# Optimization experiments

Hardware: AMD Instinct MI355X
Metric: run time of the kernel (lower is better)

The kernel has to match this reference:

```python
import jax, jax.numpy as jnp
import numpy as np

N, E, D, C, NEG_SLOPE = 50000, 800000, 128, 40, 0.2


def setup_inputs() -> dict:
    key = jax.random.key(0)
    ks = jax.random.split(key, 20)
    inp = {
        'x': jax.random.normal(ks[0], (N, D), dtype=jnp.float32),
        'edge_index': jax.random.randint(ks[1], (2, E), 0, N, dtype=jnp.int64),
    }
    s = 1.0 / np.sqrt(D)
    for l in range(3):
        inp[f'W{l}'] = jax.random.normal(ks[2 + 4 * l], (D, D), dtype=jnp.float32) * s
        inp[f'a_src{l}'] = jax.random.normal(ks[3 + 4 * l], (D,), dtype=jnp.float32) * s
        inp[f'a_dst{l}'] = jax.random.normal(ks[4 + 4 * l], (D,), dtype=jnp.float32) * s
        inp[f'b{l}'] = jnp.zeros((D,), dtype=jnp.float32)
    inp['W_head'] = jax.random.normal(ks[14], (D, C), dtype=jnp.float32) * s
    inp['b_head'] = jnp.zeros((C,), dtype=jnp.float32)
    return inp


def gat_layer(x, src, dst, W, a_src, a_dst, b):
    # x: [N, D]; src/dst: [E+N] (self-loops included)
    h = x @ W                                   # [N, D] node transform
    e_s = h @ a_src                             # [N] source attention logits
    e_d = h @ a_dst                             # [N] dest attention logits
    alpha = jax.nn.leaky_relu(e_s[src] + e_d[dst], NEG_SLOPE)  # [E+N]
    # segment softmax over incoming edges of each dst node
    m = jax.ops.segment_max(alpha, dst, num_segments=N)
    ex = jnp.exp(alpha - m[dst])
    z = jax.ops.segment_sum(ex, dst, num_segments=N)
    w = ex / z[dst]                             # [E+N] normalized attention
    out = jax.ops.segment_sum(w[:, None] * h[src], dst, num_segments=N)
    return out + b


def reference(x, edge_index, W0, a_src0, a_dst0, b0, W1, a_src1, a_dst1, b1,
              W2, a_src2, a_dst2, b2, W_head, b_head):
    loops = jnp.arange(N, dtype=edge_index.dtype)
    src = jnp.concatenate([edge_index[0], loops])  # PyG add_self_loops=True
    dst = jnp.concatenate([edge_index[1], loops])
    for W, a_s, a_d, b in ((W0, a_src0, a_dst0, b0),
                           (W1, a_src1, a_dst1, b1),
                           (W2, a_src2, a_dst2, b2)):
        x = jax.nn.relu(gat_layer(x, src, dst, W, a_s, a_d, b))
        # dropout is identity in eval mode
    return x @ W_head + b_head
```

## Files before the change

kernel.cpp:

```cpp
#include <hip/hip_runtime.h>
#include <hip/hip_bf16.h>

#define NN 50000
#define EE 800000
#define DD 128
#define CC 40
#define NEG 0.2f
#define NPAD 50048
#define NB 782
#define CEDGES 2048
#define NSCAT 391
#define PADCAP 2048
#define DEGCAP 64

typedef _Float16 half8 __attribute__((ext_vector_type(8)));
typedef unsigned short ushort8 __attribute__((ext_vector_type(8)));
typedef float floatx4 __attribute__((ext_vector_type(4)));

__device__ __forceinline__ float lrelu(float a) { return a > 0.f ? a : NEG * a; }
__device__ __forceinline__ float bf2f(unsigned short u) {
    union { unsigned int i; float f; } v; v.i = (unsigned int)u << 16; return v.f;
}

__device__ __forceinline__ int edge_at(const void* ei, int i64, long long idx) {
    return i64 ? (int)((const long long*)ei)[idx] : ((const int*)ei)[idx];
}

struct ParamCvt {
    const void* src[11];
    int off[11];
    int total;
};

__global__ __launch_bounds__(256) void prep_kernel(ParamCvt a,
                                                   const void* __restrict__ x_raw,
                                                   const void* __restrict__ ei,
                                                   const void* __restrict__ W0,
                                                   const void* __restrict__ W1,
                                                   const void* __restrict__ W2,
                                                   int* __restrict__ flags,
                                                   int* __restrict__ cursor,
                                                   unsigned int* __restrict__ pairs,
                                                   float* __restrict__ params,
                                                   _Float16* __restrict__ wpack) {
    __shared__ int cnt[NB];
    __shared__ int loff[NB];
    __shared__ int gbase[NB];
    __shared__ unsigned int lp[CEDGES];
    __shared__ int wsum[4];
    __shared__ int carry;
    int t = threadIdx.x, lane = t & 63, wid = t >> 6;
    if (blockIdx.x < NSCAT) {
        unsigned int hi0 = ((const unsigned int*)ei)[2 * lane + 1];
        int i64 = (__ballot(hi0 != 0u) == 0ull) ? 1 : 0;
        for (int i = t; i < NB; i += 256) cnt[i] = 0;
        if (t == 0) carry = 0;
        __syncthreads();
        int base = blockIdx.x * CEDGES;
        int sreg[8], dreg[8];
        #pragma unroll
        for (int j = 0; j < 8; ++j) {
            int e = base + j * 256 + t;
            if (e < EE) {
                sreg[j] = edge_at(ei, i64, e);
                dreg[j] = edge_at(ei, i64, (long long)EE + e);
                atomicAdd(&cnt[dreg[j] >> 6], 1);
            } else { sreg[j] = -1; dreg[j] = -1; }
        }
        __syncthreads();
        for (int c0 = 0; c0 < NB; c0 += 256) {
            int i = c0 + t;
            int v = (i < NB) ? cnt[i] : 0;
            int x = v;
            #pragma unroll
            for (int o = 1; o < 64; o <<= 1) {
                int y = __shfl_up(x, o, 64);
                if (lane >= o) x += y;
            }
            if (lane == 63) wsum[wid] = x;
            __syncthreads();
            int carr = carry;
            int woff = 0;
            for (int w = 0; w < wid; ++w) woff += wsum[w];
            if (i < NB) loff[i] = carr + woff + x - v;
            __syncthreads();
            if (t == 0) carry = carr + wsum[0] + wsum[1] + wsum[2] + wsum[3];
            __syncthreads();
        }
        for (int i = t; i < NB; i += 256) {
            int c = cnt[i];
            gbase[i] = c ? atomicAdd(&cursor[i], c) : 0;
        }
        __syncthreads();
        for (int i = t; i < NB; i += 256) cnt[i] = loff[i];
        __syncthreads();
        #pragma unroll
        for (int j = 0; j < 8; ++j) {
            if (dreg[j] >= 0) {
                int slot = atomicAdd(&cnt[dreg[j] >> 6], 1);
                lp[slot] = ((unsigned int)dreg[j] << 16) | (unsigned int)sreg[j];
            }
        }
        __syncthreads();
        int total = (EE - base < CEDGES) ? (EE - base) : CEDGES;
        for (int i = t; i < total; i += 256) {
            unsigned int pr = lp[i];
            int b = (int)(pr >> 22);
            int idx = gbase[b] + (i - loff[b]);
            if (idx < PADCAP)
                __builtin_nontemporal_store(pr, &pairs[(size_t)b * PADCAP + idx]);
        }
        return;
    }
    int cb = blockIdx.x - NSCAT;
    unsigned short u = ((const unsigned short*)x_raw)[lane * 2];
    int e = (u >> 7) & 0xFF;
    int bad = (!(e >= 96 && e <= 158) && u != 0 && u != 0x8000) ? 1 : 0;
    int bf = (__ballot(bad) == 0ull) ? 1 : 0;
    if (cb == 217) {
        unsigned int hi = ((const unsigned int*)ei)[2 * lane + 1];
        int i64 = (__ballot(hi != 0u) == 0ull) ? 1 : 0;
        if (t == 0) { flags[0] = bf; flags[1] = i64; }
        return;
    }
    if (cb < 192) {
        int i = cb * 256 + t;
        int l = i >> 14, r = i & 16383;
        int j = r & 7, ln = (r >> 3) & 63, ks = (r >> 9) & 3, c = r >> 11;
        int k = ks * 32 + (ln >> 4) * 8 + j;
        int ncol = c * 16 + (ln & 15);
        const void* W = (l == 0) ? W0 : ((l == 1) ? W1 : W2);
        float v = bf ? bf2f(((const unsigned short*)W)[k * 128 + ncol])
                     : ((const float*)W)[k * 128 + ncol];
        wpack[i] = (_Float16)v;
    } else {
        int i = (cb - 192) * 256 + t;
        if (i >= a.total) return;
        int k = 0;
        #pragma unroll
        for (int j = 1; j < 11; ++j) if (i >= a.off[j]) k = j;
        int local = i - a.off[k];
        params[i] = bf ? bf2f(((const unsigned short*)a.src[k])[local])
                       : ((const float*)a.src[k])[local];
    }
}

__device__ __forceinline__ void gemm_core(const half8 a[4], const _Float16* __restrict__ lw,
                                          const float* __restrict__ asrc,
                                          const float* __restrict__ adst,
                                          _Float16* __restrict__ H,
                                          float* __restrict__ es, float* __restrict__ ed,
                                          int n, int rowbase, int lane) {
    int quad = lane >> 4, col = lane & 15;
    float esp[4] = {0, 0, 0, 0}, edp[4] = {0, 0, 0, 0};
    #pragma unroll
    for (int c = 0; c < 8; ++c) {
        floatx4 acc = {0.f, 0.f, 0.f, 0.f};
        #pragma unroll
        for (int ks = 0; ks < 4; ++ks) {
            half8 b = *(const half8*)&lw[(((c * 4 + ks) * 64) + lane) * 8];
            acc = __builtin_amdgcn_mfma_f32_16x16x32_f16(a[ks], b, acc, 0, 0, 0);
        }
        float av = asrc[c * 16 + col], dv = adst[c * 16 + col];
        #pragma unroll
        for (int r = 0; r < 4; ++r) {
            int rowg = rowbase + quad * 4 + r;
            if (rowg < n) H[(size_t)rowg * 128 + c * 16 + col] = (_Float16)acc[r];
            esp[r] += acc[r] * av;
            edp[r] += acc[r] * dv;
        }
    }
    #pragma unroll
    for (int r = 0; r < 4; ++r) {
        float s = esp[r], d = edp[r];
        #pragma unroll
        for (int o = 1; o < 16; o <<= 1) {
            s += __shfl_xor(s, o, 64);
            d += __shfl_xor(d, o, 64);
        }
        int rowg = rowbase + quad * 4 + r;
        if (col == 0 && rowg < n) { es[rowg] = s; ed[rowg] = d; }
    }
}

__device__ __forceinline__ void agg_body(const _Float16* __restrict__ H,
                                         const int* __restrict__ cnt,
                                         const unsigned short* __restrict__ csr,
                                         const float* __restrict__ es,
                                         const float* __restrict__ ed,
                                         const float* __restrict__ bias,
                                         _Float16* __restrict__ Xout,
                                         int n, int blk64, int t) {
    int sub = t & 15, g = t >> 4;
    int f0 = sub * 8;
    #pragma unroll 1
    for (int r = 0; r < 4; ++r) {
        int node = blk64 + r * 16 + g;
        if (node >= n) continue;
        int total = cnt[node];
        size_t beg = (size_t)node << 6;
        float edi = ed[node];
        float wself = __expf(lrelu(es[node] + edi));
        float z = wself;
        half8 hs = *(const half8*)&H[(size_t)node * 128 + f0];
        float acc[8];
        #pragma unroll
        for (int j = 0; j < 8; ++j) acc[j] = wself * (float)hs[j];
        for (int base = 0; base < total; base += 8) {
            ushort8 c8 = *(const ushort8*)&csr[beg + base];
            int sdx[8];
            #pragma unroll
            for (int d = 0; d < 8; ++d)
                sdx[d] = (base + d < total) ? (int)c8[d] : node;
            half8 h[8];
            #pragma unroll
            for (int d = 0; d < 8; ++d)
                h[d] = *(const half8*)&H[(size_t)sdx[d] * 128 + f0];
            float wd[8];
            #pragma unroll
            for (int d = 0; d < 8; ++d) {
                float ee = __expf(lrelu(es[sdx[d]] + edi));
                wd[d] = (base + d < total) ? ee : 0.f;
                z += wd[d];
            }
            #pragma unroll
            for (int d = 0; d < 8; ++d) {
                #pragma unroll
                for (int j = 0; j < 8; ++j) acc[j] += wd[d] * (float)h[d][j];
            }
        }
        float invz = 1.f / z;
        half8 o8;
        #pragma unroll
        for (int j = 0; j < 8; ++j)
            o8[j] = (_Float16)fmaxf(acc[j] * invz + bias[f0 + j], 0.f);
        *(half8*)&Xout[(size_t)node * 128 + f0] = o8;
    }
}

__global__ __launch_bounds__(256) void bucketD_gemm0(const unsigned int* __restrict__ pairs,
                                                     const int* __restrict__ cursor,
                                                     int* __restrict__ cnt,
                                                     unsigned short* __restrict__ csr,
                                                     const void* __restrict__ Xraw,
                                                     const int* __restrict__ flags,
                                                     const _Float16* __restrict__ Wp,
                                                     const float* __restrict__ asrc,
                                                     const float* __restrict__ adst,
                                                     _Float16* __restrict__ H,
                                                     float* __restrict__ es,
                                                     float* __restrict__ ed, int n) {
    __shared__ _Float16 lw[16384];
    __shared__ int curS[64];
    int t = threadIdx.x;
    if (blockIdx.x < NB) {
        unsigned short* lcsr = (unsigned short*)lw;
        if (t < 64) curS[t] = 0;
        __syncthreads();
        int b = blockIdx.x;
        int cntb = cursor[b];
        if (cntb > PADCAP) cntb = PADCAP;
        int pbeg = b * PADCAP;
        for (int i = t; i < cntb; i += 256) {
            unsigned int pr = pairs[pbeg + i];
            int nd = (pr >> 16) & 63;
            int p = atomicAdd(&curS[nd], 1);
            if (p < DEGCAP) lcsr[nd * 64 + p] = (unsigned short)(pr & 0xFFFF);
        }
        __syncthreads();
        if (t < 64) {
            int gid = b * 64 + t;
            if (gid < NN) {
                int v = curS[t];
                cnt[gid] = v > DEGCAP ? DEGCAP : v;
            }
        }
        for (int i = t; i < 512; i += 256)
            __builtin_nontemporal_store(((const ushort8*)lcsr)[i],
                                        &((ushort8*)csr)[(size_t)b * 512 + i]);
        return;
    }
    int gb = blockIdx.x - NB;
    for (int i = t; i < 2048; i += 256)
        ((half8*)lw)[i] = ((const half8*)Wp)[i];
    int w = t >> 6, lane = t & 63;
    int quad = lane >> 4, col = lane & 15;
    int rowbase = gb * 64 + w * 16;
    half8 a[4];
    int bf = flags[0];
    int row = rowbase + col;
    if (row >= n) row = n - 1;
    if (bf) {
        const unsigned short* xr = (const unsigned short*)Xraw + (size_t)row * 128 + quad * 8;
        #pragma unroll
        for (int ks = 0; ks < 4; ++ks) {
            ushort8 u = *(const ushort8*)(xr + ks * 32);
            #pragma unroll
            for (int j = 0; j < 8; ++j) a[ks][j] = (_Float16)bf2f(u[j]);
        }
    } else {
        const float* xr = (const float*)Xraw + (size_t)row * 128 + quad * 8;
        #pragma unroll
        for (int ks = 0; ks < 4; ++ks) {
            float4 f0 = *(const float4*)(xr + ks * 32);
            float4 f1 = *(const float4*)(xr + ks * 32 + 4);
            a[ks][0] = (_Float16)f0.x; a[ks][1] = (_Float16)f0.y;
            a[ks][2] = (_Float16)f0.z; a[ks][3] = (_Float16)f0.w;
            a[ks][4] = (_Float16)f1.x; a[ks][5] = (_Float16)f1.y;
            a[ks][6] = (_Float16)f1.z; a[ks][7] = (_Float16)f1.w;
        }
    }
    __syncthreads();
    gemm_core(a, lw, asrc, adst, H, es, ed, n, rowbase, lane);
}

__global__ __launch_bounds__(256) void fused_ag(const _Float16* __restrict__ Hin,
                                                const int* __restrict__ cnt,
                                                const unsigned short* __restrict__ csr,
                                                const float* __restrict__ esin,
                                                const float* __restrict__ edin,
                                                const float* __restrict__ bias,
                                                _Float16* __restrict__ X,
                                                const _Float16* __restrict__ Wp,
                                                const float* __restrict__ asrc,
                                                const float* __restrict__ adst,
                                                _Float16* __restrict__ Hout,
                                                float* __restrict__ esout,
                                                float* __restrict__ edout, int n) {
    __shared__ _Float16 lw[16384];
    int t = threadIdx.x;
    for (int i = t; i < 2048; i += 256)
        ((half8*)lw)[i] = ((const half8*)Wp)[i];
    agg_body(Hin, cnt, csr, esin, edin, bias, X, n, blockIdx.x * 64, t);
    __syncthreads();
    int w = t >> 6, lane = t & 63;
    int quad = lane >> 4, col = lane & 15;
    int rowbase = blockIdx.x * 64 + w * 16;
    int row = rowbase + col;
    if (row >= n) row = n - 1;
    half8 a[4];
    const _Float16* xrow = X + (size_t)row * 128 + quad * 8;
    #pragma unroll
    for (int ks = 0; ks < 4; ++ks) a[ks] = *(const half8*)(xrow + ks * 32);
    gemm_core(a, lw, asrc, adst, Hout, esout, edout, n, rowbase, lane);
}

__global__ __launch_bounds__(256) void fused_ah(const _Float16* __restrict__ Hin,
                                                const int* __restrict__ cnt,
                                                const unsigned short* __restrict__ csr,
                                                const float* __restrict__ esin,
                                                const float* __restrict__ edin,
                                                const float* __restrict__ bias,
                                                _Float16* __restrict__ X,
                                                const float* __restrict__ Whf,
                                                const float* __restrict__ bhf,
                                                const int* __restrict__ flags,
                                                void* __restrict__ out, int n) {
    __shared__ float ws[128 * 40];
    __shared__ float xs[64 * 129];
    int t = threadIdx.x;
    for (int i = t; i < 128 * 40; i += 256) ws[i] = Whf[i];
    agg_body(Hin, cnt, csr, esin, edin, bias, X, n, blockIdx.x * 64, t);
    __syncthreads();
    int bm = blockIdx.x * 64;
    for (int i = t; i < 64 * 16; i += 256) {
        int r = i >> 4, c8 = i & 15;
        half8 v = *(const half8*)&X[(size_t)(bm + r) * 128 + c8 * 8];
        #pragma unroll
        for (int j = 0; j < 8; ++j) xs[r * 129 + c8 * 8 + j] = (float)v[j];
    }
    __syncthreads();
    int r = t >> 2, cg = t & 3;
    int c0 = cg * 10;
    float acc[10] = {};
    for (int k = 0; k < 128; ++k) {
        float xr = xs[r * 129 + k];
        #pragma unroll
        for (int j = 0; j < 10; ++j) acc[j] += xr * ws[k * 40 + c0 + j];
    }
    int row = bm + r;
    if (row < n) {
        if (flags[0]) {
            __hip_bfloat16* ob = (__hip_bfloat16*)out;
            #pragma unroll
            for (int j = 0; j < 10; ++j)
                ob[row * 40 + c0 + j] = __float2bfloat16(acc[j] + bhf[c0 + j]);
        } else {
            float* of = (float*)out;
            #pragma unroll
            for (int j = 0; j < 10; ++j)
                of[row * 40 + c0 + j] = acc[j] + bhf[c0 + j];
        }
    }
}

extern "C" void kernel_launch(void* const* d_in, const int* in_sizes, int n_in,
                              void* d_out, int out_size, void* d_ws, size_t ws_size,
                              hipStream_t stream) {
    const void* x_raw = d_in[0];
    const void* ei    = d_in[1];

    char* p = (char*)d_ws;
    auto alloc = [&](size_t bytes) { void* r = (void*)p; p += (bytes + 255) & ~(size_t)255; return r; };
    int*            flags  = (int*)alloc(16);
    _Float16*       X      = (_Float16*)alloc((size_t)NPAD * DD * 2);
    _Float16*       H0     = (_Float16*)alloc((size_t)NPAD * DD * 2);
    _Float16*       H1     = (_Float16*)alloc((size_t)NPAD * DD * 2);
    float*          es0    = (float*)alloc((size_t)NN * 4);
    float*          ed0    = (float*)alloc((size_t)NN * 4);
    float*          es1    = (float*)alloc((size_t)NN * 4);
    float*          ed1    = (float*)alloc((size_t)NN * 4);
    int*            cnt    = (int*)alloc((size_t)NN * 4);
    unsigned short* csr    = (unsigned short*)alloc((size_t)NB * 4096 * 2);
    unsigned int*   pairs  = (unsigned int*)alloc((size_t)NB * PADCAP * 4);
    int*            cursor = (int*)alloc((size_t)NB * 4);
    _Float16*       wpack  = (_Float16*)alloc((size_t)3 * 16384 * 2);
    float*          params = (float*)alloc((size_t)(3 * 384 + 5160) * 4);

    ParamCvt pc;
    {
        int k = 0, off = 0;
        auto add = [&](const void* s, int nel) { pc.src[k] = s; pc.off[k] = off; off += nel; ++k; };
        for (int l = 0; l < 3; ++l) {
            add(d_in[3 + 4 * l], 128);
            add(d_in[4 + 4 * l], 128);
            add(d_in[5 + 4 * l], 128);
        }
        add(d_in[14], 5120);
        add(d_in[15], 40);
        pc.total = off;
    }

    hipMemsetAsync(cursor, 0, (size_t)NB * 4, stream);
    prep_kernel<<<NSCAT + 218, 256, 0, stream>>>(pc, x_raw, ei, d_in[2], d_in[6], d_in[10],
                                                 flags, cursor, pairs, params, wpack);

    const int ngb = NPAD / 64;
    float* base0 = params;
    float* base1 = params + 384;
    float* base2 = params + 768;
    bucketD_gemm0<<<NB + ngb, 256, 0, stream>>>(pairs, cursor, cnt, csr,
                                                x_raw, flags, wpack, base0, base0 + 128,
                                                H0, es0, ed0, NN);
    fused_ag<<<ngb, 256, 0, stream>>>(H0, cnt, csr, es0, ed0, base0 + 256, X,
                                      wpack + 16384, base1, base1 + 128,
                                      H1, es1, ed1, NN);
    fused_ag<<<ngb, 256, 0, stream>>>(H1, cnt, csr, es1, ed1, base1 + 256, X,
                                      wpack + 32768, base2, base2 + 128,
                                      H0, es0, ed0, NN);
    fused_ah<<<ngb, 256, 0, stream>>>(H0, cnt, csr, es0, ed0, base2 + 256, X,
                                      params + 1152, params + 1152 + 5120, flags, d_out, NN);
}
```

Measured before the change: 278.1 us.

## Keep aggregated features in LDS and read packed weights from global

The aggregation output now goes into a per-block shared-memory tile instead of a global X buffer, and the following GEMM (or head projection) reads it straight from LDS. This removes a global write and read-back of the full feature matrix per layer. The packed weight matrix is no longer staged into 32KB of LDS; MFMA B operands are loaded directly from global/L2, which cuts LDS use and one sync but puts weight loads in the inner loop. The head kernel also drops its float conversion staging buffer.

After: 272.2 us. 2.1% less time.

```diff
diff --git a/kernel.cpp b/kernel.cpp
--- a/kernel.cpp
+++ b/kernel.cpp
@@ -145,7 +145,7 @@
     }
 }
 
-__device__ __forceinline__ void gemm_core(const half8 a[4], const _Float16* __restrict__ lw,
+__device__ __forceinline__ void gemm_core(const half8 a[4], const _Float16* __restrict__ Wg,
                                           const float* __restrict__ asrc,
                                           const float* __restrict__ adst,
                                           _Float16* __restrict__ H,
@@ -158,7 +158,7 @@
         floatx4 acc = {0.f, 0.f, 0.f, 0.f};
         #pragma unroll
         for (int ks = 0; ks < 4; ++ks) {
-            half8 b = *(const half8*)&lw[(((c * 4 + ks) * 64) + lane) * 8];
+            half8 b = *(const half8*)&Wg[(((c * 4 + ks) * 64) + lane) * 8];
             acc = __builtin_amdgcn_mfma_f32_16x16x32_f16(a[ks], b, acc, 0, 0, 0);
         }
         float av = asrc[c * 16 + col], dv = adst[c * 16 + col];
@@ -189,7 +189,7 @@
                                          const float* __restrict__ es,
                                          const float* __restrict__ ed,
                                          const float* __restrict__ bias,
-                                         _Float16* __restrict__ Xout,
+                                         _Float16* __restrict__ xt,
                                          int n, int blk64, int t) {
     int sub = t & 15, g = t >> 4;
     int f0 = sub * 8;
@@ -234,7 +234,7 @@
         #pragma unroll
         for (int j = 0; j < 8; ++j)
             o8[j] = (_Float16)fmaxf(acc[j] * invz + bias[f0 + j], 0.f);
-        *(half8*)&Xout[(size_t)node * 128 + f0] = o8;
+        *(half8*)&xt[(size_t)(r * 16 + g) * 128 + f0] = o8;
     }
 }
 
@@ -250,11 +250,10 @@
                                                      _Float16* __restrict__ H,
                                                      float* __restrict__ es,
                                                      float* __restrict__ ed, int n) {
-    __shared__ _Float16 lw[16384];
+    __shared__ unsigned short lcsr[4096];
     __shared__ int curS[64];
     int t = threadIdx.x;
     if (blockIdx.x < NB) {
-        unsigned short* lcsr = (unsigned short*)lw;
         if (t < 64) curS[t] = 0;
         __syncthreads();
         int b = blockIdx.x;
@@ -281,8 +280,6 @@
         return;
     }
     int gb = blockIdx.x - NB;
-    for (int i = t; i < 2048; i += 256)
-        ((half8*)lw)[i] = ((const half8*)Wp)[i];
     int w = t >> 6, lane = t & 63;
     int quad = lane >> 4, col = lane & 15;
     int rowbase = gb * 64 + w * 16;
@@ -310,8 +307,7 @@
             a[ks][6] = (_Float16)f1.z; a[ks][7] = (_Float16)f1.w;
         }
     }
-    __syncthreads();
-    gemm_core(a, lw, asrc, adst, H, es, ed, n, rowbase, lane);
+    gemm_core(a, Wp, asrc, adst, H, es, ed, n, rowbase, lane);
 }
 
 __global__ __launch_bounds__(256) void fused_ag(const _Float16* __restrict__ Hin,
@@ -320,29 +316,25 @@
                                                 const float* __restrict__ esin,
                                                 const float* __restrict__ edin,
                                                 const float* __restrict__ bias,
-                                                _Float16* __restrict__ X,
                                                 const _Float16* __restrict__ Wp,
                                                 const float* __restrict__ asrc,
                                                 const float* __restrict__ adst,
                                                 _Float16* __restrict__ Hout,
                                                 float* __restrict__ esout,
                                                 float* __restrict__ edout, int n) {
-    __shared__ _Float16 lw[16384];
+    __shared__ _Float16 xt[64 * 128];
     int t = threadIdx.x;
-    for (int i = t; i < 2048; i += 256)
-        ((half8*)lw)[i] = ((const half8*)Wp)[i];
-    agg_body(Hin, cnt, csr, esin, edin, bias, X, n, blockIdx.x * 64, t);
+    agg_body(Hin, cnt, csr, esin, edin, bias, xt, n, blockIdx.x * 64, t);
     __syncthreads();
     int w = t >> 6, lane = t & 63;
     int quad = lane >> 4, col = lane & 15;
     int rowbase = blockIdx.x * 64 + w * 16;
-    int row = rowbase + col;
-    if (row >= n) row = n - 1;
+    int rl = w * 16 + col;
     half8 a[4];
-    const _Float16* xrow = X + (size_t)row * 128 + quad * 8;
     #pragma unroll
-    for (int ks = 0; ks < 4; ++ks) a[ks] = *(const half8*)(xrow + ks * 32);
-    gemm_core(a, lw, asrc, adst, Hout, esout, edout, n, rowbase, lane);
+    for (int ks = 0; ks < 4; ++ks)
+        a[ks] = *(const half8*)&xt[(size_t)rl * 128 + ks * 32 + quad * 8];
+    gemm_core(a, Wp, asrc, adst, Hout, esout, edout, n, rowbase, lane);
 }
 
 __global__ __launch_bounds__(256) void fused_ah(const _Float16* __restrict__ Hin,
@@ -351,34 +343,32 @@
                                                 const float* __restrict__ esin,
                                                 const float* __restrict__ edin,
                                                 const float* __restrict__ bias,
-                                                _Float16* __restrict__ X,
                                                 const float* __restrict__ Whf,
                                                 const float* __restrict__ bhf,
                                                 const int* __restrict__ flags,
                                                 void* __restrict__ out, int n) {
+    __shared__ _Float16 xt[64 * 128];
     __shared__ float ws[128 * 40];
-    __shared__ float xs[64 * 129];
     int t = threadIdx.x;
-    for (int i = t; i < 128 * 40; i += 256) ws[i] = Whf[i];
-    agg_body(Hin, cnt, csr, esin, edin, bias, X, n, blockIdx.x * 64, t);
-    __syncthreads();
-    int bm = blockIdx.x * 64;
-    for (int i = t; i < 64 * 16; i += 256) {
-        int r = i >> 4, c8 = i & 15;
-        half8 v = *(const half8*)&X[(size_t)(bm + r) * 128 + c8 * 8];
-        #pragma unroll
-        for (int j = 0; j < 8; ++j) xs[r * 129 + c8 * 8 + j] = (float)v[j];
-    }
+    for (int i = t; i < 1280; i += 256)
+        ((float4*)ws)[i] = ((const float4*)Whf)[i];
+    agg_body(Hin, cnt, csr, esin, edin, bias, xt, n, blockIdx.x * 64, t);
     __syncthreads();
     int r = t >> 2, cg = t & 3;
     int c0 = cg * 10;
     float acc[10] = {};
-    for (int k = 0; k < 128; ++k) {
-        float xr = xs[r * 129 + k];
-        #pragma unroll
-        for (int j = 0; j < 10; ++j) acc[j] += xr * ws[k * 40 + c0 + j];
-    }
-    int row = bm + r;
+    #pragma unroll 4
+    for (int kb = 0; kb < 16; ++kb) {
+        half8 x8 = *(const half8*)&xt[(size_t)r * 128 + kb * 8];
+        #pragma unroll
+        for (int j8 = 0; j8 < 8; ++j8) {
+            float xr = (float)x8[j8];
+            int k = kb * 8 + j8;
+            #pragma unroll
+            for (int j = 0; j < 10; ++j) acc[j] += xr * ws[k * 40 + c0 + j];
+        }
+    }
+    int row = blockIdx.x * 64 + r;
     if (row < n) {
         if (flags[0]) {
             __hip_bfloat16* ob = (__hip_bfloat16*)out;
@@ -403,7 +393,6 @@
     char* p = (char*)d_ws;
     auto alloc = [&](size_t bytes) { void* r = (void*)p; p += (bytes + 255) & ~(size_t)255; return r; };
     int*            flags  = (int*)alloc(16);
-    _Float16*       X      = (_Float16*)alloc((size_t)NPAD * DD * 2);
     _Float16*       H0     = (_Float16*)alloc((size_t)NPAD * DD * 2);
     _Float16*       H1     = (_Float16*)alloc((size_t)NPAD * DD * 2);
     float*          es0    = (float*)alloc((size_t)NN * 4);
@@ -442,12 +431,12 @@
     bucketD_gemm0<<<NB + ngb, 256, 0, stream>>>(pairs, cursor, cnt, csr,
                                                 x_raw, flags, wpack, base0, base0 + 128,
                                                 H0, es0, ed0, NN);
-    fused_ag<<<ngb, 256, 0, stream>>>(H0, cnt, csr, es0, ed0, base0 + 256, X,
+    fused_ag<<<ngb, 256, 0, stream>>>(H0, cnt, csr, es0, ed0, base0 + 256,
                                       wpack + 16384, base1, base1 + 128,
                                       H1, es1, ed1, NN);
-    fused_ag<<<ngb, 256, 0, stream>>>(H1, cnt, csr, es1, ed1, base1 + 256, X,
+    fused_ag<<<ngb, 256, 0, stream>>>(H1, cnt, csr, es1, ed1, base1 + 256,
                                       wpack + 32768, base2, base2 + 128,
                                       H0, es0, ed0, NN);
-    fused_ah<<<ngb, 256, 0, stream>>>(H0, cnt, csr, es0, ed0, base2 + 256, X,
+    fused_ah<<<ngb, 256, 0, stream>>>(H0, cnt, csr, es0, ed0, base2 + 256,
                                       params + 1152, params + 1152 + 5120, flags, d_out, NN);
 }
```
